# Kernel optimization log

Hardware: AMD Instinct MI355X
Metric: run time of the kernel (lower is better)

Reference implementation:

```python
import jax, jax.numpy as jnp
import numpy as np

N_NODES = 10000
N_EDGES = 160000
DIM = 1024


def setup_inputs() -> dict:
    key = jax.random.key(0)
    k1, k2, k3 = jax.random.split(key, 3)
    x = jax.random.normal(k1, (N_NODES, DIM), dtype=jnp.float32)
    edge_index = jax.random.randint(k2, (2, N_EDGES), 0, N_NODES, dtype=jnp.int64)
    # Glorot-style init for the GCNConv weight; zero bias (PyG default)
    W = jax.random.normal(k3, (DIM, DIM), dtype=jnp.float32) * (1.0 / np.sqrt(DIM))
    b = jnp.zeros((DIM,), dtype=jnp.float32)
    return {"x": x, "edge_index": edge_index, "W": W, "b": b}


def reference(x, edge_index, W, b):
    """GCNConv (add_self_loops=True, symmetric norm) -> Dropout(eval=identity) -> ReLU."""
    n = x.shape[0]
    loops = jnp.arange(n, dtype=edge_index.dtype)
    src = jnp.concatenate([edge_index[0], loops])  # [E+N]
    dst = jnp.concatenate([edge_index[1], loops])  # [E+N]

    # symmetric normalization: deg^{-1/2}[src] * deg^{-1/2}[dst], deg on dst side
    deg = jax.ops.segment_sum(jnp.ones_like(dst, dtype=x.dtype), dst, num_segments=n)
    dinv = jnp.where(deg > 0, jax.lax.rsqrt(deg), jnp.zeros_like(deg))
    norm = dinv[src] * dinv[dst]  # [E+N]

    h = x @ W                                   # [N, D] dense transform first
    msg = h[src] * norm[:, None]                # gather + edge scaling [E+N, D]
    out = jax.ops.segment_sum(msg, dst, num_segments=n) + b  # scatter-add + bias

    # Dropout(0.5) is identity in eval mode; activation is ReLU
    return jax.nn.relu(out)
```

## Files before the change

### kernel.cpp

```cpp
#include <hip/hip_runtime.h>
#include <hip/hip_bf16.h>
#include <cstdint>
#include <cstddef>

typedef __bf16 bf16x8 __attribute__((ext_vector_type(8)));
typedef float  f32x4  __attribute__((ext_vector_type(4)));
typedef float  f32x2  __attribute__((ext_vector_type(2)));

#define D_DIM 1024
#define BM 128
#define BN 128
#define NXCD 8
#define CAP 64

#define GLB(p) ((const __attribute__((address_space(1))) void*)(p))
#define LDS(p) ((__attribute__((address_space(3))) void*)(p))

__global__ __launch_bounds__(256) void prep_kernel(
    const float* __restrict__ x, __bf16* __restrict__ xb,
    const float* __restrict__ W, __bf16* __restrict__ wT,
    const int* __restrict__ ei, int* __restrict__ cnt, int* __restrict__ col,
    int N, int MP, int E, int nconv, int ntr)
{
    int blk = blockIdx.x, tid = threadIdx.x;
    if (blk < nconv) {
        int i = blk * 256 + tid;
        int total = MP * (D_DIM / 8);
        if (i >= total) return;
        int row = i >> 7;
        size_t base = (size_t)i * 8;
        bf16x8 o;
        if (row < N) {
            float4 v0 = *(const float4*)(x + base);
            float4 v1 = *(const float4*)(x + base + 4);
            o[0] = (__bf16)v0.x; o[1] = (__bf16)v0.y; o[2] = (__bf16)v0.z; o[3] = (__bf16)v0.w;
            o[4] = (__bf16)v1.x; o[5] = (__bf16)v1.y; o[6] = (__bf16)v1.z; o[7] = (__bf16)v1.w;
        } else {
            #pragma unroll
            for (int j = 0; j < 8; ++j) o[j] = (__bf16)0.f;
        }
        *(bf16x8*)(xb + base) = o;
    } else if (blk < nconv + ntr) {
        __shared__ float tile[32][33];
        int bb = blk - nconv;
        int nb = (bb & 31) * 32, kb = (bb >> 5) * 32;
        int tx = tid & 31, ty = tid >> 5;
        #pragma unroll
        for (int i = 0; i < 32; i += 8)
            tile[ty + i][tx] = W[(size_t)(kb + ty + i) * D_DIM + nb + tx];
        __syncthreads();
        #pragma unroll
        for (int i = 0; i < 32; i += 8)
            wT[(size_t)(nb + ty + i) * D_DIM + kb + tx] = (__bf16)tile[tx][ty + i];
    } else {
        int e = (blk - nconv - ntr) * 256 + tid;
        if (e < E) {
            const int* src = ei;
            const int* dst = ei + E;
            int d = dst[e];
            int pos = atomicAdd(&cnt[d], 1);
            if (pos < CAP) col[(d << 6) + pos] = src[e] << 11;
        }
    }
}

__global__ __launch_bounds__(256) void gemmpad_kernel(
    const __bf16* __restrict__ A,
    const __bf16* __restrict__ BT,
    __bf16* __restrict__ C,
    const int* __restrict__ cnt, int* __restrict__ col, int Nn,
    int mtiles, int ntiles, int chunk, int npad)
{
    int tid = threadIdx.x;
    if ((int)blockIdx.x < npad) {
        int d = blockIdx.x * 256 + tid;
        if (d < Nn) {
            int c  = min(cnt[d], CAP);
            int p1 = (c + 7) & ~7;
            int zoff = Nn << 11;
            for (int p = c; p < p1; ++p) col[(d << 6) + p] = zoff;
        }
        return;
    }
    __shared__ __bf16 As[2][BM * 32];
    __shared__ __bf16 Bs[2][BN * 32];

    int wg = blockIdx.x - npad;
    int c8 = wg & (NXCD - 1);
    int r  = wg >> 3;
    int bm = c8 * chunk + r / ntiles;
    int bn = r % ntiles;
    if (bm >= mtiles) return;

    int wid = tid >> 6, lane = tid & 63;
    int wr = wid >> 1, wc = wid & 1;

    auto stage = [&](int h, int sel) {
        #pragma unroll
        for (int i = 0; i < 2; ++i) {
            int c   = i * 256 + tid;
            int row = c >> 2;
            int js  = (c & 3) ^ ((row ^ (row >> 2)) & 3);
            const __bf16* ga = A  + (size_t)(bm * BM + row) * D_DIM + h * 32 + js * 8;
            const __bf16* gb = BT + (size_t)(bn * BN + row) * D_DIM + h * 32 + js * 8;
            __builtin_amdgcn_global_load_lds(GLB(ga), LDS(&As[sel][c * 8]), 16, 0, 0);
            __builtin_amdgcn_global_load_lds(GLB(gb), LDS(&Bs[sel][c * 8]), 16, 0, 0);
        }
    };

    f32x4 acc[4][4] = {};
    stage(0, 0);
    asm volatile("s_waitcnt vmcnt(0)" ::: "memory");
    __syncthreads();

    const int halves = D_DIM / 32;
    for (int h = 0; h < halves; ++h) {
        int cur = h & 1;
        if (h + 1 < halves) stage(h + 1, cur ^ 1);
        bf16x8 af[4], bfr[4];
        int j = lane >> 4;
        #pragma unroll
        for (int mi = 0; mi < 4; ++mi) {
            int rr = wr * 64 + mi * 16 + (lane & 15);
            int sw = (rr ^ (rr >> 2)) & 3;
            af[mi] = *(const bf16x8*)(&As[cur][rr * 32 + ((j ^ sw) << 3)]);
        }
        #pragma unroll
        for (int ni = 0; ni < 4; ++ni) {
            int rr = wc * 64 + ni * 16 + (lane & 15);
            int sw = (rr ^ (rr >> 2)) & 3;
            bfr[ni] = *(const bf16x8*)(&Bs[cur][rr * 32 + ((j ^ sw) << 3)]);
        }
        #pragma unroll
        for (int mi = 0; mi < 4; ++mi)
            #pragma unroll
            for (int ni = 0; ni < 4; ++ni)
                acc[mi][ni] = __builtin_amdgcn_mfma_f32_16x16x32_bf16(
                    af[mi], bfr[ni], acc[mi][ni], 0, 0, 0);
        __syncthreads();
    }

    #pragma unroll
    for (int mi = 0; mi < 4; ++mi)
        #pragma unroll
        for (int rr = 0; rr < 4; ++rr) {
            int row = bm * BM + wr * 64 + mi * 16 + (lane >> 4) * 4 + rr;
            float dvr = 0.0f;
            if (row < Nn) dvr = rsqrtf((float)min(cnt[row], CAP) + 1.0f);
            #pragma unroll
            for (int ni = 0; ni < 4; ++ni) {
                int colc = bn * BN + wc * 64 + ni * 16 + (lane & 15);
                C[(size_t)row * D_DIM + colc] = (__bf16)(acc[mi][ni][rr] * dvr);
            }
        }
}

__global__ __launch_bounds__(256) void scatter_kernel(
    const __bf16* __restrict__ h, const int* __restrict__ cnt,
    const int* __restrict__ col, const float* __restrict__ bias,
    float* __restrict__ out, int N)
{
    int blk = blockIdx.x;
    int c   = blk & (NXCD - 1);
    int q   = blk >> 3;
    int wid = threadIdx.x >> 6, lane = threadIdx.x & 63;
    int d = q * 4 + wid;
    if (d >= N) return;

    const char* hb = (const char*)h + (size_t)c * 256;
    int lane4 = lane * 4;

    uint32_t su = *(const uint32_t*)(hb + (((uint32_t)d << 11) + lane4));
    f32x2 a;
    a[0] = __uint_as_float(su << 16);
    a[1] = __uint_as_float(su & 0xffff0000u);

    int cdeg = min(cnt[d], CAP);
    int r0 = d << 6;
    int r1 = r0 + ((cdeg + 7) & ~7);
    for (int e = r0; e < r1; e += 8) {
        int4 c0 = *(const int4*)(col + e);
        int4 c1 = *(const int4*)(col + e + 4);
        uint32_t u[8];
        u[0] = *(const uint32_t*)(hb + ((uint32_t)c0.x + lane4));
        u[1] = *(const uint32_t*)(hb + ((uint32_t)c0.y + lane4));
        u[2] = *(const uint32_t*)(hb + ((uint32_t)c0.z + lane4));
        u[3] = *(const uint32_t*)(hb + ((uint32_t)c0.w + lane4));
        u[4] = *(const uint32_t*)(hb + ((uint32_t)c1.x + lane4));
        u[5] = *(const uint32_t*)(hb + ((uint32_t)c1.y + lane4));
        u[6] = *(const uint32_t*)(hb + ((uint32_t)c1.z + lane4));
        u[7] = *(const uint32_t*)(hb + ((uint32_t)c1.w + lane4));
        #pragma unroll
        for (int t = 0; t < 8; ++t) {
            f32x2 v;
            v[0] = __uint_as_float(u[t] << 16);
            v[1] = __uint_as_float(u[t] & 0xffff0000u);
            a += v;
        }
    }

    float dv = rsqrtf((float)cdeg + 1.0f);
    int cbase = c * 128 + lane * 2;
    f32x2 bb = *(const f32x2*)(bias + cbase);
    f32x2 o;
    o[0] = fmaxf(fmaf(a[0], dv, bb[0]), 0.f);
    o[1] = fmaxf(fmaf(a[1], dv, bb[1]), 0.f);
    __builtin_nontemporal_store(o, (f32x2*)(out + (size_t)d * D_DIM + cbase));
}

extern "C" void kernel_launch(void* const* d_in, const int* in_sizes, int n_in,
                              void* d_out, int out_size, void* d_ws, size_t ws_size,
                              hipStream_t stream)
{
    const float* x  = (const float*)d_in[0];
    const int*   ei = (const int*)d_in[1];
    const float* W  = (const float*)d_in[2];
    const float* b  = (const float*)d_in[3];
    float* out = (float*)d_out;

    const int N = in_sizes[0] / D_DIM;
    const int E = in_sizes[1] / 2;
    const int MP = ((N + BM - 1) / BM) * BM;

    char* ws = (char*)d_ws;
    size_t off = 0;
    auto alloc = [&](size_t bytes) -> char* {
        char* p = ws + off;
        off += (bytes + 255) & ~(size_t)255;
        return p;
    };
    __bf16* xb  = (__bf16*)alloc((size_t)MP * D_DIM * 2);
    __bf16* wT  = (__bf16*)alloc((size_t)D_DIM * D_DIM * 2);
    __bf16* h   = (__bf16*)alloc((size_t)MP * D_DIM * 2);
    int*    cnt = (int*)alloc((size_t)N * 4);
    int*    col = (int*)alloc((size_t)N * CAP * 4);
    (void)ws_size;

    (void)hipMemsetAsync(cnt, 0, (size_t)N * 4, stream);

    int nconv = (MP * (D_DIM / 8) + 255) / 256;
    int ntr   = (D_DIM / 32) * (D_DIM / 32);
    int ncnt  = (E + 255) / 256;
    prep_kernel<<<nconv + ntr + ncnt, 256, 0, stream>>>(x, xb, W, wT, ei,
                                                        cnt, col, N, MP, E,
                                                        nconv, ntr);

    int mtiles = MP / BM;
    int ntiles = D_DIM / BN;
    int chunk  = (mtiles + NXCD - 1) / NXCD;
    int ngem   = NXCD * chunk * ntiles;
    int npad   = (N + 255) / 256;
    gemmpad_kernel<<<npad + ngem, 256, 0, stream>>>(xb, wT, h, cnt, col, N,
                                                    mtiles, ntiles, chunk, npad);

    int sblocks = ((N + 3) / 4) * NXCD;
    scatter_kernel<<<sblocks, 256, 0, stream>>>(h, cnt, col, b, out, N);
}
```

Measured before the change: 101.3 us.

## Fuse fp32-to-bf16 conversion of x into GEMM A-tile loading

Removes the separate conversion of x to a bf16 workspace in the prep kernel; the GEMM now loads fp32 rows of x into registers, converts to bf16 and writes swizzled LDS tiles, while B still uses direct global-to-LDS loads. The main loop is restructured into explicit ping-pong over two LDS buffers with loads issued before compute. This avoids a full write and re-read of the bf16 copy of x, but each GEMM block now reads twice as many bytes of x and routes them through registers instead of async LDS loads.

Measured after the change: 157.6 us. +55.5%, slower.

```diff
diff --git a/kernel.cpp b/kernel.cpp
--- a/kernel.cpp
+++ b/kernel.cpp
@@ -17,33 +17,14 @@
 #define LDS(p) ((__attribute__((address_space(3))) void*)(p))
 
 __global__ __launch_bounds__(256) void prep_kernel(
-    const float* __restrict__ x, __bf16* __restrict__ xb,
     const float* __restrict__ W, __bf16* __restrict__ wT,
     const int* __restrict__ ei, int* __restrict__ cnt, int* __restrict__ col,
-    int N, int MP, int E, int nconv, int ntr)
+    int N, int E, int ntr)
 {
     int blk = blockIdx.x, tid = threadIdx.x;
-    if (blk < nconv) {
-        int i = blk * 256 + tid;
-        int total = MP * (D_DIM / 8);
-        if (i >= total) return;
-        int row = i >> 7;
-        size_t base = (size_t)i * 8;
-        bf16x8 o;
-        if (row < N) {
-            float4 v0 = *(const float4*)(x + base);
-            float4 v1 = *(const float4*)(x + base + 4);
-            o[0] = (__bf16)v0.x; o[1] = (__bf16)v0.y; o[2] = (__bf16)v0.z; o[3] = (__bf16)v0.w;
-            o[4] = (__bf16)v1.x; o[5] = (__bf16)v1.y; o[6] = (__bf16)v1.z; o[7] = (__bf16)v1.w;
-        } else {
-            #pragma unroll
-            for (int j = 0; j < 8; ++j) o[j] = (__bf16)0.f;
-        }
-        *(bf16x8*)(xb + base) = o;
-    } else if (blk < nconv + ntr) {
+    if (blk < ntr) {
         __shared__ float tile[32][33];
-        int bb = blk - nconv;
-        int nb = (bb & 31) * 32, kb = (bb >> 5) * 32;
+        int nb = (blk & 31) * 32, kb = (blk >> 5) * 32;
         int tx = tid & 31, ty = tid >> 5;
         #pragma unroll
         for (int i = 0; i < 32; i += 8)
@@ -53,7 +34,7 @@
         for (int i = 0; i < 32; i += 8)
             wT[(size_t)(nb + ty + i) * D_DIM + kb + tx] = (__bf16)tile[tx][ty + i];
     } else {
-        int e = (blk - nconv - ntr) * 256 + tid;
+        int e = (blk - ntr) * 256 + tid;
         if (e < E) {
             const int* src = ei;
             const int* dst = ei + E;
@@ -65,7 +46,7 @@
 }
 
 __global__ __launch_bounds__(256) void gemmpad_kernel(
-    const __bf16* __restrict__ A,
+    const float* __restrict__ X,
     const __bf16* __restrict__ BT,
     __bf16* __restrict__ C,
     const int* __restrict__ cnt, int* __restrict__ col, int Nn,
@@ -95,48 +76,102 @@
     int wid = tid >> 6, lane = tid & 63;
     int wr = wid >> 1, wc = wid & 1;
 
-    auto stage = [&](int h, int sel) {
-        #pragma unroll
-        for (int i = 0; i < 2; ++i) {
-            int c   = i * 256 + tid;
-            int row = c >> 2;
-            int js  = (c & 3) ^ ((row ^ (row >> 2)) & 3);
-            const __bf16* ga = A  + (size_t)(bm * BM + row) * D_DIM + h * 32 + js * 8;
-            const __bf16* gb = BT + (size_t)(bn * BN + row) * D_DIM + h * 32 + js * 8;
-            __builtin_amdgcn_global_load_lds(GLB(ga), LDS(&As[sel][c * 8]), 16, 0, 0);
-            __builtin_amdgcn_global_load_lds(GLB(gb), LDS(&Bs[sel][c * 8]), 16, 0, 0);
-        }
+    int ar = tid >> 1;
+    int ag = tid & 1;
+    int rowg = bm * BM + ar;
+    bool aval = rowg < Nn;
+    const float* xp = X + (size_t)rowg * D_DIM + ag * 16;
+    int asw   = (ar ^ (ar >> 2)) & 3;
+    int widx0 = ar * 32 + ((((ag << 1))     ^ asw) << 3);
+    int widx1 = ar * 32 + ((((ag << 1) | 1) ^ asw) << 3);
+
+    const __bf16* gbp[2];
+    int bofs[2];
+    #pragma unroll
+    for (int i = 0; i < 2; ++i) {
+        int c   = i * 256 + tid;
+        int row = c >> 2;
+        int js  = (c & 3) ^ ((row ^ (row >> 2)) & 3);
+        gbp[i]  = BT + (size_t)(bn * BN + row) * D_DIM + js * 8;
+        bofs[i] = c * 8;
+    }
+
+    int j = lane >> 4;
+    int offA[4], offB[4];
+    #pragma unroll
+    for (int mi = 0; mi < 4; ++mi) {
+        int rr = wr * 64 + mi * 16 + (lane & 15);
+        offA[mi] = rr * 32 + ((j ^ ((rr ^ (rr >> 2)) & 3)) << 3);
+    }
+    #pragma unroll
+    for (int ni = 0; ni < 4; ++ni) {
+        int rr = wc * 64 + ni * 16 + (lane & 15);
+        offB[ni] = rr * 32 + ((j ^ ((rr ^ (rr >> 2)) & 3)) << 3);
+    }
+
+    float4 av0, av1, av2, av3;
+    auto loadA = [&](int h) {
+        if (aval) {
+            const float* p = xp + h * 32;
+            av0 = *(const float4*)(p);
+            av1 = *(const float4*)(p + 4);
+            av2 = *(const float4*)(p + 8);
+            av3 = *(const float4*)(p + 12);
+        } else {
+            av0 = av1 = av2 = av3 = float4{0.f, 0.f, 0.f, 0.f};
+        }
+    };
+    auto writeA = [&](__bf16* Ab) {
+        bf16x8 o0, o1;
+        o0[0] = (__bf16)av0.x; o0[1] = (__bf16)av0.y;
+        o0[2] = (__bf16)av0.z; o0[3] = (__bf16)av0.w;
+        o0[4] = (__bf16)av1.x; o0[5] = (__bf16)av1.y;
+        o0[6] = (__bf16)av1.z; o0[7] = (__bf16)av1.w;
+        o1[0] = (__bf16)av2.x; o1[1] = (__bf16)av2.y;
+        o1[2] = (__bf16)av2.z; o1[3] = (__bf16)av2.w;
+        o1[4] = (__bf16)av3.x; o1[5] = (__bf16)av3.y;
+        o1[6] = (__bf16)av3.z; o1[7] = (__bf16)av3.w;
+        *(bf16x8*)(Ab + widx0) = o0;
+        *(bf16x8*)(Ab + widx1) = o1;
+    };
+    auto stageB = [&](int h, __bf16* Bb) {
+        __builtin_amdgcn_global_load_lds(GLB(gbp[0] + h * 32), LDS(Bb + bofs[0]), 16, 0, 0);
+        __builtin_amdgcn_global_load_lds(GLB(gbp[1] + h * 32), LDS(Bb + bofs[1]), 16, 0, 0);
     };
 
     f32x4 acc[4][4] = {};
-    stage(0, 0);
-    asm volatile("s_waitcnt vmcnt(0)" ::: "memory");
-    __syncthreads();
-
-    const int halves = D_DIM / 32;
-    for (int h = 0; h < halves; ++h) {
-        int cur = h & 1;
-        if (h + 1 < halves) stage(h + 1, cur ^ 1);
+    auto compute = [&](const __bf16* Ab, const __bf16* Bb) {
         bf16x8 af[4], bfr[4];
-        int j = lane >> 4;
-        #pragma unroll
-        for (int mi = 0; mi < 4; ++mi) {
-            int rr = wr * 64 + mi * 16 + (lane & 15);
-            int sw = (rr ^ (rr >> 2)) & 3;
-            af[mi] = *(const bf16x8*)(&As[cur][rr * 32 + ((j ^ sw) << 3)]);
-        }
-        #pragma unroll
-        for (int ni = 0; ni < 4; ++ni) {
-            int rr = wc * 64 + ni * 16 + (lane & 15);
-            int sw = (rr ^ (rr >> 2)) & 3;
-            bfr[ni] = *(const bf16x8*)(&Bs[cur][rr * 32 + ((j ^ sw) << 3)]);
-        }
+        #pragma unroll
+        for (int mi = 0; mi < 4; ++mi) af[mi] = *(const bf16x8*)(Ab + offA[mi]);
+        #pragma unroll
+        for (int ni = 0; ni < 4; ++ni) bfr[ni] = *(const bf16x8*)(Bb + offB[ni]);
         #pragma unroll
         for (int mi = 0; mi < 4; ++mi)
             #pragma unroll
             for (int ni = 0; ni < 4; ++ni)
                 acc[mi][ni] = __builtin_amdgcn_mfma_f32_16x16x32_bf16(
                     af[mi], bfr[ni], acc[mi][ni], 0, 0, 0);
+    };
+
+    loadA(0);
+    stageB(0, Bs[0]);
+    asm volatile("s_waitcnt vmcnt(0)" ::: "memory");
+    writeA(As[0]);
+    __syncthreads();
+
+    for (int h = 0; h < 32; h += 2) {
+        loadA(h + 1);
+        stageB(h + 1, Bs[1]);
+        compute(As[0], Bs[0]);
+        asm volatile("s_waitcnt vmcnt(0)" ::: "memory");
+        writeA(As[1]);
+        __syncthreads();
+        bool more = (h + 2) < 32;
+        if (more) { loadA(h + 2); stageB(h + 2, Bs[0]); }
+        compute(As[1], Bs[1]);
+        asm volatile("s_waitcnt vmcnt(0)" ::: "memory");
+        if (more) writeA(As[0]);
         __syncthreads();
     }
 
@@ -229,7 +264,6 @@
         off += (bytes + 255) & ~(size_t)255;
         return p;
     };
-    __bf16* xb  = (__bf16*)alloc((size_t)MP * D_DIM * 2);
     __bf16* wT  = (__bf16*)alloc((size_t)D_DIM * D_DIM * 2);
     __bf16* h   = (__bf16*)alloc((size_t)MP * D_DIM * 2);
     int*    cnt = (int*)alloc((size_t)N * 4);
@@ -238,19 +272,16 @@
 
     (void)hipMemsetAsync(cnt, 0, (size_t)N * 4, stream);
 
-    int nconv = (MP * (D_DIM / 8) + 255) / 256;
-    int ntr   = (D_DIM / 32) * (D_DIM / 32);
-    int ncnt  = (E + 255) / 256;
-    prep_kernel<<<nconv + ntr + ncnt, 256, 0, stream>>>(x, xb, W, wT, ei,
-                                                        cnt, col, N, MP, E,
-                                                        nconv, ntr);
+    int ntr  = (D_DIM / 32) * (D_DIM / 32);
+    int ncnt = (E + 255) / 256;
+    prep_kernel<<<ntr + ncnt, 256, 0, stream>>>(W, wT, ei, cnt, col, N, E, ntr);
 
     int mtiles = MP / BM;
     int ntiles = D_DIM / BN;
     int chunk  = (mtiles + NXCD - 1) / NXCD;
     int ngem   = NXCD * chunk * ntiles;
     int npad   = (N + 255) / 256;
-    gemmpad_kernel<<<npad + ngem, 256, 0, stream>>>(xb, wT, h, cnt, col, N,
+    gemmpad_kernel<<<npad + ngem, 256, 0, stream>>>(x, wT, h, cnt, col, N,
                                                     mtiles, ntiles, chunk, npad);
 
     int sblocks = ((N + 3) / 4) * NXCD;
```
